# Performance work log

Measured on AMD Instinct MI355X. Metric: run time of the kernel, lower is better.

The kernel has to match this reference:

```python
import jax, jax.numpy as jnp
import numpy as np


def _project(feat, x, y):
    """Bilinear sample feat [H,W,C] at float coords (x along H, y along W) -> [N,C]."""
    H, W, _ = feat.shape
    x1 = jnp.floor(x)
    x2 = jnp.minimum(jnp.ceil(x), H - 1.0)
    y1 = jnp.floor(y)
    y2 = jnp.minimum(jnp.ceil(y), W - 1.0)
    xi1, xi2 = x1.astype(jnp.int32), x2.astype(jnp.int32)
    yi1, yi2 = y1.astype(jnp.int32), y2.astype(jnp.int32)
    Q11 = feat[xi1, yi1]  # [N,C]
    Q12 = feat[xi1, yi2]
    Q21 = feat[xi2, yi1]
    Q22 = feat[xi2, yi2]
    w11 = ((x2 - x) * (y2 - y))[:, None]
    w21 = ((x - x1) * (y2 - y))[:, None]
    w12 = ((x2 - x) * (y - y1))[:, None]
    w22 = ((x - x1) * (y - y1))[:, None]
    return w11 * Q11 + w21 * Q21 + w12 * Q12 + w22 * Q22


def setup_inputs() -> dict:
    key = jax.random.key(0)
    k0, k1, k2, k3, k4, k5 = jax.random.split(key, 6)
    N = 100000
    xy = jax.random.normal(k0, (N, 2), dtype=jnp.float32) * 0.5
    # Z must be strictly negative for the perspective division by -Z
    z = -(jax.random.uniform(k5, (N, 1), dtype=jnp.float32) * 2.0 + 0.5)
    coords = jnp.concatenate([xy, z], axis=1)
    feat1 = jax.random.normal(k1, (56, 56, 64), dtype=jnp.float32)
    feat2 = jax.random.normal(k2, (28, 28, 128), dtype=jnp.float32)
    feat3 = jax.random.normal(k3, (14, 14, 256), dtype=jnp.float32)
    feat4 = jax.random.normal(k4, (7, 7, 512), dtype=jnp.float32)
    return {"coords": coords, "feat1": feat1, "feat2": feat2,
            "feat3": feat3, "feat4": feat4}


def reference(coords, feat1, feat2, feat3, feat4):
    X = coords[:, 0]
    Y = coords[:, 1]
    Z = coords[:, 2]
    h = 250.0 * (-Y) / (-Z) + 112.0
    w = 250.0 * X / (-Z) + 112.0
    h = jnp.clip(h, 0.0, 223.0)
    w = jnp.clip(w, 0.0, 223.0)
    outs = [coords]
    for feat, size in ((feat1, 56.0), (feat2, 28.0), (feat3, 14.0), (feat4, 7.0)):
        x = h / (224.0 / size)
        y = w / (224.0 / size)
        outs.append(_project(feat, x, y))
    return jnp.concatenate(outs, axis=1)  # [N, 3+64+128+256+512]
```

## Files before the change

### kernel.cpp

```cpp
#include <hip/hip_runtime.h>


#define ROWF 963

template<int H, int C, int CHBASE>
__device__ __forceinline__ void do_level(
    const float* __restrict__ f, float h, float w,
    float* __restrict__ orow, int lane)
{
    const float scale = (float)H / 224.0f;
    const float x = h * scale, y = w * scale;
    const float x1f = floorf(x), x2f = fminf(ceilf(x), (float)(H - 1));
    const float y1f = floorf(y), y2f = fminf(ceilf(y), (float)(H - 1));
    const int xi1 = (int)x1f, xi2 = (int)x2f;
    const int yi1 = (int)y1f, yi2 = (int)y2f;

    const float w11 = (x2f - x) * (y2f - y);
    const float w21 = (x - x1f) * (y2f - y);
    const float w12 = (x2f - x) * (y - y1f);
    const float w22 = (x - x1f) * (y - y1f);

    const float* q11 = f + __builtin_amdgcn_readfirstlane((xi1 * H + yi1) * C);
    const float* q21 = f + __builtin_amdgcn_readfirstlane((xi2 * H + yi1) * C);
    const float* q12 = f + __builtin_amdgcn_readfirstlane((xi1 * H + yi2) * C);
    const float* q22 = f + __builtin_amdgcn_readfirstlane((xi2 * H + yi2) * C);

    #pragma unroll
    for (int k = 0; k < C / 64; ++k) {
        const int c = lane + 64 * k;
        orow[CHBASE + c] = w11 * q11[c] + w21 * q21[c]
                         + w12 * q12[c] + w22 * q22[c];
    }
}

__global__ __launch_bounds__(256) void graphproj_kernel(
    const float* __restrict__ coords,
    const float* __restrict__ f1, const float* __restrict__ f2,
    const float* __restrict__ f3, const float* __restrict__ f4,
    float* __restrict__ out, int N)
{
    const int lane = threadIdx.x & 63;
    const int wv   = __builtin_amdgcn_readfirstlane(threadIdx.x >> 6);
    const int p    = blockIdx.x * 4 + wv;
    if (p >= N) return;

    const float X = coords[p * 3 + 0];
    const float Y = coords[p * 3 + 1];
    const float Z = coords[p * 3 + 2];

    float h = 250.0f * (-Y) / (-Z) + 112.0f;
    float w = 250.0f * X / (-Z) + 112.0f;
    h = fminf(fmaxf(h, 0.0f), 223.0f);
    w = fminf(fmaxf(w, 0.0f), 223.0f);

    float* orow = out + (size_t)p * ROWF + 3;

    if (lane < 3) {
        out[(size_t)p * ROWF + lane] = (lane == 0) ? X : (lane == 1) ? Y : Z;
    }

    do_level<56,  64,   0>(f1, h, w, orow, lane);
    do_level<28, 128,  64>(f2, h, w, orow, lane);
    do_level<14, 256, 192>(f3, h, w, orow, lane);
    do_level< 7, 512, 448>(f4, h, w, orow, lane);
}

extern "C" void kernel_launch(void* const* d_in, const int* in_sizes, int n_in,
                              void* d_out, int out_size, void* d_ws, size_t ws_size,
                              hipStream_t stream) {
    const float* coords = (const float*)d_in[0];
    const float* f1 = (const float*)d_in[1];
    const float* f2 = (const float*)d_in[2];
    const float* f3 = (const float*)d_in[3];
    const float* f4 = (const float*)d_in[4];
    float* out = (float*)d_out;
    const int N = in_sizes[0] / 3;

    const int blocks = (N + 3) / 4;
    graphproj_kernel<<<blocks, 256, 0, stream>>>(coords, f1, f2, f3, f4, out, N);
}
```

Measured before the change: 88.18 us.

## Stage level-4 feature map in LDS with persistent 1024-thread blocks and nontemporal stores

Each 1024-thread block first copies the whole 7x7x512 level-4 feature map (about 100 KB) into shared memory. Its 16 waves then loop over 400 points, sampling level 4 from LDS instead of global memory. Output writes become nontemporal stores so the large streaming output does not pollute the cache. The cost is a per-block 100 KB copy, which with 250 blocks adds redundant global traffic and a sync before any work starts. The large LDS footprint also allows only one block per CU.

```diff
diff --git a/kernel.cpp b/kernel.cpp
--- a/kernel.cpp
+++ b/kernel.cpp
@@ -1,10 +1,15 @@
 #include <hip/hip_runtime.h>
 
 
-#define ROWF 963
+#define ROWF    963
+#define PPB     400
+#define THREADS 1024
+#define F4SZ    (7 * 7 * 512)
+
+typedef float fx4 __attribute__((ext_vector_type(4)));
 
 template<int H, int C, int CHBASE>
-__device__ __forceinline__ void do_level(
+__device__ __forceinline__ void do_level_global(
     const float* __restrict__ f, float h, float w,
     float* __restrict__ orow, int lane)
 {
@@ -28,41 +33,85 @@
     #pragma unroll
     for (int k = 0; k < C / 64; ++k) {
         const int c = lane + 64 * k;
-        orow[CHBASE + c] = w11 * q11[c] + w21 * q21[c]
-                         + w12 * q12[c] + w22 * q22[c];
+        const float v = w11 * q11[c] + w21 * q21[c]
+                      + w12 * q12[c] + w22 * q22[c];
+        __builtin_nontemporal_store(v, &orow[CHBASE + c]);
     }
 }
 
-__global__ __launch_bounds__(256) void graphproj_kernel(
+__global__ __launch_bounds__(THREADS) void graphproj_kernel(
     const float* __restrict__ coords,
     const float* __restrict__ f1, const float* __restrict__ f2,
     const float* __restrict__ f3, const float* __restrict__ f4,
     float* __restrict__ out, int N)
 {
-    const int lane = threadIdx.x & 63;
-    const int wv   = __builtin_amdgcn_readfirstlane(threadIdx.x >> 6);
-    const int p    = blockIdx.x * 4 + wv;
-    if (p >= N) return;
+    __shared__ float s_f4[F4SZ];
 
-    const float X = coords[p * 3 + 0];
-    const float Y = coords[p * 3 + 1];
-    const float Z = coords[p * 3 + 2];
+    const int tid = threadIdx.x;
 
-    float h = 250.0f * (-Y) / (-Z) + 112.0f;
-    float w = 250.0f * X / (-Z) + 112.0f;
-    h = fminf(fmaxf(h, 0.0f), 223.0f);
-    w = fminf(fmaxf(w, 0.0f), 223.0f);
+    {
+        const fx4* __restrict__ src = (const fx4*)f4;
+        fx4* dst = (fx4*)s_f4;
+        #pragma unroll 1
+        for (int i = tid; i < F4SZ / 4; i += THREADS) dst[i] = src[i];
+    }
+    __syncthreads();
 
-    float* orow = out + (size_t)p * ROWF + 3;
+    const int lane  = tid & 63;
+    const int wid   = __builtin_amdgcn_readfirstlane(tid >> 6);
+    const int pbase = blockIdx.x * PPB;
 
-    if (lane < 3) {
-        out[(size_t)p * ROWF + lane] = (lane == 0) ? X : (lane == 1) ? Y : Z;
+    #pragma unroll 1
+    for (int j = 0; j < PPB / 16; ++j) {
+        const int p = pbase + wid + j * 16;
+        if (p >= N) break;
+
+        const float X = coords[p * 3 + 0];
+        const float Y = coords[p * 3 + 1];
+        const float Z = coords[p * 3 + 2];
+
+        float h = 250.0f * (-Y) / (-Z) + 112.0f;
+        float w = 250.0f * X / (-Z) + 112.0f;
+        h = fminf(fmaxf(h, 0.0f), 223.0f);
+        w = fminf(fmaxf(w, 0.0f), 223.0f);
+
+        float* orow = out + (size_t)p * ROWF + 3;
+
+        if (lane < 3) {
+            out[(size_t)p * ROWF + lane] = (lane == 0) ? X : (lane == 1) ? Y : Z;
+        }
+
+        do_level_global<56,  64,   0>(f1, h, w, orow, lane);
+        do_level_global<28, 128,  64>(f2, h, w, orow, lane);
+        do_level_global<14, 256, 192>(f3, h, w, orow, lane);
+
+        {
+            const float scale = 7.0f / 224.0f;
+            const float x = h * scale, y = w * scale;
+            const float x1f = floorf(x), x2f = fminf(ceilf(x), 6.0f);
+            const float y1f = floorf(y), y2f = fminf(ceilf(y), 6.0f);
+            const int xi1 = (int)x1f, xi2 = (int)x2f;
+            const int yi1 = (int)y1f, yi2 = (int)y2f;
+
+            const float w11 = (x2f - x) * (y2f - y);
+            const float w21 = (x - x1f) * (y2f - y);
+            const float w12 = (x2f - x) * (y - y1f);
+            const float w22 = (x - x1f) * (y - y1f);
+
+            const int o11 = (xi1 * 7 + yi1) * 512;
+            const int o21 = (xi2 * 7 + yi1) * 512;
+            const int o12 = (xi1 * 7 + yi2) * 512;
+            const int o22 = (xi2 * 7 + yi2) * 512;
+
+            #pragma unroll
+            for (int k = 0; k < 8; ++k) {
+                const int c = lane + 64 * k;
+                const float v = w11 * s_f4[o11 + c] + w21 * s_f4[o21 + c]
+                              + w12 * s_f4[o12 + c] + w22 * s_f4[o22 + c];
+                __builtin_nontemporal_store(v, &orow[448 + c]);
+            }
+        }
     }
-
-    do_level<56,  64,   0>(f1, h, w, orow, lane);
-    do_level<28, 128,  64>(f2, h, w, orow, lane);
-    do_level<14, 256, 192>(f3, h, w, orow, lane);
-    do_level< 7, 512, 448>(f4, h, w, orow, lane);
 }
 
 extern "C" void kernel_launch(void* const* d_in, const int* in_sizes, int n_in,
@@ -76,6 +125,6 @@
     float* out = (float*)d_out;
     const int N = in_sizes[0] / 3;
 
-    const int blocks = (N + 3) / 4;
-    graphproj_kernel<<<blocks, 256, 0, stream>>>(coords, f1, f2, f3, f4, out, N);
+    const int blocks = (N + PPB - 1) / PPB;
+    graphproj_kernel<<<blocks, THREADS, 0, stream>>>(coords, f1, f2, f3, f4, out, N);
 }
```

Result: slower. 136.6 us (+54.9%).
